# Kernel optimization log

Measured on AMD Instinct MI355X. Metric: run time of the kernel, lower is better.

## Reference

```python
import jax, jax.numpy as jnp
import numpy as np

NUM_USERS = 50000
NUM_ITEMS = 50000
NUM_CATS = 500
LATENT_DIM = 64
N_LAYERS = 3
N_EDGES = 500000
NNZ_G = 1000000
NNZ_GX = 2000000
BATCH = 8192
N_NODES = NUM_USERS + NUM_ITEMS


def _spmm(rows, cols, vals, x, n_out):
    # sparse COO matmul: out[r] += vals * x[c]
    return jax.ops.segment_sum(vals[:, None] * x[cols], rows, num_segments=n_out)


def setup_inputs() -> dict:
    key = jax.random.key(0)
    ks = jax.random.split(key, 14)
    return {
        "user_emb": 0.1 * jax.random.normal(ks[0], (NUM_USERS, LATENT_DIM), jnp.float32),
        "item_emb": 0.1 * jax.random.normal(ks[1], (NUM_ITEMS, LATENT_DIM), jnp.float32),
        "cat_emb": 0.1 * jax.random.normal(ks[2], (NUM_CATS, 2 * LATENT_DIM), jnp.float32),
        "g_vals": jax.random.uniform(ks[3], (NNZ_G,), jnp.float32),
        "gx_vals": jax.random.uniform(ks[4], (NNZ_GX,), jnp.float32),
        "g_rows": jax.random.randint(ks[5], (NNZ_G,), 0, N_NODES, jnp.int32),
        "g_cols": jax.random.randint(ks[6], (NNZ_G,), 0, N_NODES, jnp.int32),
        "gx_rows": jax.random.randint(ks[7], (NNZ_GX,), 0, N_EDGES, jnp.int32),
        "gx_cols": jax.random.randint(ks[8], (NNZ_GX,), 0, N_EDGES, jnp.int32),
        "train_users": jax.random.randint(ks[9], (N_EDGES,), 0, NUM_USERS, jnp.int32),
        "train_items": jax.random.randint(ks[10], (N_EDGES,), 0, NUM_ITEMS, jnp.int32),
        "item_to_category": jax.random.randint(ks[11], (NUM_ITEMS,), 0, NUM_CATS, jnp.int32),
        "users": jax.random.randint(ks[12], (BATCH,), 0, NUM_USERS, jnp.int32),
        "items": jax.random.randint(ks[13], (BATCH,), 0, NUM_ITEMS, jnp.int32),
    }


def _computer(user_emb, item_emb, cat_emb, g_rows, g_cols, g_vals,
              gx_rows, gx_cols, gx_vals, train_users, train_items, item_to_category):
    D = LATENT_DIM
    all_emb = jnp.concatenate([user_emb, item_emb], axis=0)  # [N, D]
    item_nodes = NUM_USERS + train_items  # [E]
    # degree = bincount over train_users and shifted train_items
    degree = (jnp.zeros((N_NODES,), all_emb.dtype)
              .at[train_users].add(1.0)
              .at[item_nodes].add(1.0))
    edge_cat = cat_emb[item_to_category[train_items]]  # [E, 2D]
    embs = []
    for i in range(N_LAYERS):
        all_emb = _spmm(g_rows, g_cols, g_vals, all_emb, N_NODES)  # [N, D]
        # edge features: user||item concat, +category emb on first layer
        feat = jnp.concatenate([all_emb[train_users], all_emb[item_nodes]], axis=-1)  # [E, 2D]
        if i == 0:
            feat = feat + edge_cat
        feat = _spmm(gx_rows, gx_cols, gx_vals, feat, N_EDGES)  # [E, 2D]
        # scatter edge halves back to nodes, degree-normalize, residual average
        upd = (jnp.zeros_like(all_emb)
               .at[train_users].add(feat[:, :D])
               .at[item_nodes].add(feat[:, D:]))
        upd = upd / (degree[:, None] + 1e-9)
        all_emb = (upd + all_emb) * 0.5
        embs.append(all_emb)
    light_out = jnp.mean(jnp.stack(embs, axis=1), axis=1)  # mean over layers 1..L
    return light_out[:NUM_USERS], light_out[NUM_USERS:]


def reference(user_emb, item_emb, cat_emb, g_vals, gx_vals, g_rows, g_cols,
              gx_rows, gx_cols, train_users, train_items, item_to_category,
              users, items):
    all_users, all_items = _computer(user_emb, item_emb, cat_emb,
                                     g_rows, g_cols, g_vals,
                                     gx_rows, gx_cols, gx_vals,
                                     train_users, train_items, item_to_category)
    u = all_users[users]   # [B, D]
    it = all_items[items]  # [B, D]
    gamma = jnp.sum(u * it, axis=1)  # [B]
    return gamma
```

## Files before the change

### kernel.cpp

```cpp
#include <hip/hip_runtime.h>

#define NUM_USERS 50000
#define NUM_ITEMS 50000
#define NUM_CATS  500
#define D         64
#define N_LAYERS  3
#define N_EDGES   500000
#define NNZ_G     1000000
#define NNZ_GX    2000000
#define BATCH     8192
#define N_NODES   (NUM_USERS + NUM_ITEMS)

#define BKT_SHIFT 4
#define BKT_W     16
#define NBKT      (N_NODES / BKT_W)

#define SB_SHIFT  9
#define SB_W      512
#define NSB       ((N_NODES + SB_W - 1) / SB_W)
#define P1_K      8
#define P1_TILE   (256 * P1_K)

__device__ __forceinline__ unsigned bf16rne(float f) {
    unsigned u = __float_as_uint(f);
    return (u + 0x7FFFu + ((u >> 16) & 1u)) >> 16;
}
__device__ __forceinline__ void bf16x8_to_f8(uint4 w, float* r) {
    r[0] = __uint_as_float(w.x << 16); r[1] = __uint_as_float(w.x & 0xFFFF0000u);
    r[2] = __uint_as_float(w.y << 16); r[3] = __uint_as_float(w.y & 0xFFFF0000u);
    r[4] = __uint_as_float(w.z << 16); r[5] = __uint_as_float(w.z & 0xFFFF0000u);
    r[6] = __uint_as_float(w.w << 16); r[7] = __uint_as_float(w.w & 0xFFFF0000u);
}
__device__ __forceinline__ uint4 f8_to_bf16x8(const float* r) {
    uint4 w;
    w.x = bf16rne(r[0]) | (bf16rne(r[1]) << 16);
    w.y = bf16rne(r[2]) | (bf16rne(r[3]) << 16);
    w.z = bf16rne(r[4]) | (bf16rne(r[5]) << 16);
    w.w = bf16rne(r[6]) | (bf16rne(r[7]) << 16);
    return w;
}

__global__ void init_deg_kernel(const float* __restrict__ ue, const float* __restrict__ ie,
                                const int* __restrict__ tu, const int* __restrict__ ti,
                                ushort* __restrict__ xb, float* __restrict__ deg) {
    int tid = blockIdx.x * blockDim.x + threadIdx.x;
    int stride = gridDim.x * blockDim.x;
    for (int e = tid; e < N_EDGES; e += stride) {
        unsafeAtomicAdd(deg + tu[e], 1.0f);
        unsafeAtomicAdd(deg + NUM_USERS + ti[e], 1.0f);
    }
    const int half = NUM_USERS * D / 4;
    for (int i4 = tid; i4 < N_NODES * D / 4; i4 += stride) {
        float4 v = (i4 < half) ? ((const float4*)ue)[i4] : ((const float4*)ie)[i4 - half];
        uint2 p;
        p.x = bf16rne(v.x) | (bf16rne(v.y) << 16);
        p.y = bf16rne(v.z) | (bf16rne(v.w) << 16);
        ((uint2*)xb)[i4] = p;
    }
}

__global__ void dinv_kernel(float* __restrict__ deg) {
    int n = blockIdx.x * blockDim.x + threadIdx.x;
    if (n < N_NODES) deg[n] = 1.0f / (deg[n] + 1e-9f);
}

__global__ void histsb_c_kernel(const int* __restrict__ gx_rows,
                                const int* __restrict__ tu, const int* __restrict__ ti,
                                int* __restrict__ cnt) {
    __shared__ int h[NSB];
    for (int i = threadIdx.x; i < NSB; i += blockDim.x) h[i] = 0;
    __syncthreads();
    int stride = gridDim.x * blockDim.x;
    for (int j = blockIdx.x * blockDim.x + threadIdx.x; j < NNZ_GX; j += stride) {
        int r = gx_rows[j];
        atomicAdd(h + (tu[r] >> SB_SHIFT), 1);
        atomicAdd(h + ((NUM_USERS + ti[r]) >> SB_SHIFT), 1);
    }
    __syncthreads();
    for (int i = threadIdx.x; i < NSB; i += blockDim.x)
        if (h[i]) atomicAdd(cnt + i, h[i]);
}

__global__ void scansb_kernel(const int* __restrict__ cnt, int* __restrict__ off,
                              int* __restrict__ cur, int* __restrict__ row_sentinel) {
    if (threadIdx.x == 0) {
        int run = 0;
        for (int i = 0; i < NSB; ++i) { off[i] = run; cur[i] = run; run += cnt[i]; }
        off[NSB] = run;
        row_sentinel[0] = run;
    }
}

__global__ void __launch_bounds__(256) p1c_kernel(
        const int* __restrict__ gx_rows, const int* __restrict__ gx_cols,
        const float* __restrict__ gx_vals,
        const int* __restrict__ tu, const int* __restrict__ ti,
        const int* __restrict__ i2c,
        int* __restrict__ sbcur, int2* __restrict__ out) {
    __shared__ int2 recs[2 * P1_TILE];
    __shared__ int h[NSB], base[NSB], cur[NSB];
    int t = threadIdx.x;
    for (int i = t; i < NSB; i += 256) { h[i] = 0; cur[i] = 0; }
    __syncthreads();
    int tb = blockIdx.x * P1_TILE;
    #pragma unroll
    for (int k = 0; k < P1_K; ++k) {
        int l = t + k * 256;
        int j = tb + l;
        if (j < NNZ_GX) {
            int r = gx_rows[j], c = gx_cols[j];
            unsigned vb = bf16rne(gx_vals[j]);
            int tur = tu[r], tir = ti[r], tuc = tu[c], tic = ti[c];
            int cat = i2c[tic];
            int ylo = (int)(vb << 16) | (cat << 1);
            unsigned dstu = (unsigned)tur;           int srcu = tuc;
            unsigned dsti = (unsigned)(NUM_USERS + tir); int srci = NUM_USERS + tic;
            recs[l] = make_int2((int)((dstu << 15) | (unsigned)(srcu & 0x7FFF)),
                                ylo | (((srcu >> 15) & 3) << 10));
            recs[P1_TILE + l] = make_int2((int)((dsti << 15) | (unsigned)(srci & 0x7FFF)),
                                          ylo | (((srci >> 15) & 3) << 10) | 1);
            atomicAdd(h + (int)(dstu >> SB_SHIFT), 1);
            atomicAdd(h + (int)(dsti >> SB_SHIFT), 1);
        }
    }
    __syncthreads();
    if (t < NSB) base[t] = atomicAdd(sbcur + t, h[t]);
    __syncthreads();
    int rem = NNZ_GX - tb;
    int nv = rem < P1_TILE ? rem : P1_TILE;
    for (int s = t; s < nv; s += 256) {
        int2 rec = recs[s];
        int bkt = (int)(((unsigned)rec.x) >> 24);
        int p = base[bkt] + atomicAdd(cur + bkt, 1);
        out[p] = rec;
        rec = recs[P1_TILE + s];
        bkt = (int)(((unsigned)rec.x) >> 24);
        p = base[bkt] + atomicAdd(cur + bkt, 1);
        out[p] = rec;
    }
}

__global__ void __launch_bounds__(512) p2c_kernel(
        const int* __restrict__ sboff, const int2* __restrict__ raw,
        int2* __restrict__ sorted, int* __restrict__ rowC) {
    int b = blockIdx.x;
    int beg = sboff[b], end = sboff[b + 1];
    __shared__ int h[SB_W], cur[SB_W];
    int t = threadIdx.x;
    h[t] = 0;
    __syncthreads();
    for (int i = beg + t; i < end; i += 512)
        atomicAdd(h + (int)((((unsigned)raw[i].x) >> 15) & (SB_W - 1)), 1);
    __syncthreads();
    int cnt = h[t];
    for (int o = 1; o < SB_W; o <<= 1) {
        int tmp = (t >= o) ? h[t - o] : 0;
        __syncthreads();
        h[t] += tmp;
        __syncthreads();
    }
    int excl = h[t] - cnt;
    cur[t] = beg + excl;
    int node = b * SB_W + t;
    if (node < N_NODES) rowC[node] = beg + excl;
    __syncthreads();
    for (int i = beg + t; i < end; i += 512) {
        int2 e = raw[i];
        unsigned rx = (unsigned)e.x;
        int dl = (int)((rx >> 15) & (SB_W - 1));
        int src = (int)(rx & 0x7FFF) | (((e.y >> 10) & 3) << 15);
        int p = atomicAdd(cur + dl, 1);
        sorted[p] = make_int2((src << 10) | (e.y & 0x3FF), e.y & 0xFFFF0000);
    }
}

__global__ void histg_kernel(const int* __restrict__ g_rows, int* __restrict__ cnt) {
    __shared__ int h[NBKT];
    for (int i = threadIdx.x; i < NBKT; i += blockDim.x) h[i] = 0;
    __syncthreads();
    int stride = gridDim.x * blockDim.x;
    for (int e = blockIdx.x * blockDim.x + threadIdx.x; e < NNZ_G; e += stride)
        atomicAdd(h + (g_rows[e] >> BKT_SHIFT), 1);
    __syncthreads();
    for (int i = threadIdx.x; i < NBKT; i += blockDim.x)
        if (h[i]) atomicAdd(cnt + i, h[i]);
}

__global__ void scang_kernel(const int* __restrict__ cnt, int* __restrict__ off,
                             int* __restrict__ cur, int* __restrict__ row) {
    __shared__ int sums[1024];
    const int T = 1024;
    const int strip = (NBKT + T - 1) / T;
    int t = threadIdx.x;
    int beg = t * strip;
    int end = beg + strip; if (end > NBKT) end = NBKT;
    int s = 0;
    for (int i = beg; i < end; ++i) s += cnt[i];
    sums[t] = s;
    __syncthreads();
    if (t == 0) {
        int run = 0;
        for (int i = 0; i < T; ++i) { int v = sums[i]; sums[i] = run; run += v; }
        off[NBKT] = run;
        row[N_NODES] = run;
    }
    __syncthreads();
    int run = sums[t];
    for (int i = beg; i < end; ++i) { off[i] = run; cur[i] = run; run += cnt[i]; }
}

__global__ void append_g_kernel(const int* __restrict__ g_rows, const int* __restrict__ g_cols,
                                const float* __restrict__ g_vals,
                                int* __restrict__ cur, int2* __restrict__ edges) {
    int e = blockIdx.x * blockDim.x + threadIdx.x;
    if (e >= NNZ_G) return;
    int dst = g_rows[e];
    int p = atomicAdd(cur + (dst >> BKT_SHIFT), 1);
    edges[p] = make_int2(((dst & (BKT_W - 1)) << 17) | g_cols[e], __float_as_int(g_vals[e]));
}

__global__ void sort_g_kernel(const int* __restrict__ off, const int2* __restrict__ raw,
                              int2* __restrict__ sorted, int* __restrict__ rowG) {
    int b = blockIdx.x;
    int base = off[b], end = off[b + 1];
    __shared__ int hist[BKT_W], cur[BKT_W], scn[BKT_W];
    if (threadIdx.x < BKT_W) hist[threadIdx.x] = 0;
    __syncthreads();
    for (int i = base + threadIdx.x; i < end; i += blockDim.x)
        atomicAdd(hist + ((raw[i].x >> 17) & 15), 1);
    __syncthreads();
    if (threadIdx.x == 0) {
        int run = 0;
        for (int k = 0; k < BKT_W; ++k) { scn[k] = run; cur[k] = run; run += hist[k]; }
    }
    __syncthreads();
    if (threadIdx.x < BKT_W) rowG[b * BKT_W + threadIdx.x] = base + scn[threadIdx.x];
    for (int i = base + threadIdx.x; i < end; i += blockDim.x) {
        int2 e = raw[i];
        int dl = (e.x >> 17) & 15;
        int p = atomicAdd(cur + dl, 1);
        sorted[base + p] = make_int2((e.x & 0x1FFFF) << 6, e.y);
    }
}

__global__ void pull_g_kernel(const int* __restrict__ row, const int2* __restrict__ edges,
                              const ushort* __restrict__ xb, ushort* __restrict__ tb) {
    int node = (blockIdx.x * blockDim.x + threadIdx.x) >> 5;
    int l32 = threadIdx.x & 31;
    if (node >= N_NODES) return;
    int g = l32 >> 3;
    int s = l32 & 7;
    int beg = row[node], end = row[node + 1];
    float acc[8] = {0.f, 0.f, 0.f, 0.f, 0.f, 0.f, 0.f, 0.f};
    #pragma unroll 2
    for (int i = beg + g; i < end; i += 4) {
        int2 e = edges[i];
        float v = __int_as_float(e.y);
        uint4 w = *(const uint4*)(xb + e.x + s * 8);
        float xv[8];
        bf16x8_to_f8(w, xv);
        #pragma unroll
        for (int d = 0; d < 8; ++d) acc[d] += v * xv[d];
    }
    #pragma unroll
    for (int d = 0; d < 8; ++d) {
        acc[d] += __shfl_xor(acc[d], 8, 64);
        acc[d] += __shfl_xor(acc[d], 16, 64);
    }
    if (l32 < 8) {
        uint4 p = f8_to_bf16x8(acc);
        *(uint4*)(tb + (size_t)node * D + s * 8) = p;
    }
}

template <int LAYER0>
__global__ void pull_c_fused(const int* __restrict__ row, const int2* __restrict__ edges,
                             const float* __restrict__ catbase,
                             const ushort* __restrict__ tb,
                             const float* __restrict__ dinv,
                             ushort* __restrict__ xout) {
    int node = (blockIdx.x * blockDim.x + threadIdx.x) >> 5;
    int l32 = threadIdx.x & 31;
    if (node >= N_NODES) return;
    int g = l32 >> 3;
    int s = l32 & 7;
    int beg = row[node], end = row[node + 1];
    float acc[8] = {0.f, 0.f, 0.f, 0.f, 0.f, 0.f, 0.f, 0.f};
    #pragma unroll 2
    for (int i = beg + g; i < end; i += 4) {
        int2 e = edges[i];
        float v = __int_as_float(e.y);
        int src = e.x >> 10;
        uint4 w = *(const uint4*)(tb + (size_t)src * D + s * 8);
        float xv[8];
        bf16x8_to_f8(w, xv);
        if (LAYER0) {
            int code = e.x & 1023;
            const float* cb = catbase + (code >> 1) * (2 * D) + ((code & 1) << 6) + s * 8;
            float4 c0 = *(const float4*)cb;
            float4 c1 = *(const float4*)(cb + 4);
            xv[0] += c0.x; xv[1] += c0.y; xv[2] += c0.z; xv[3] += c0.w;
            xv[4] += c1.x; xv[5] += c1.y; xv[6] += c1.z; xv[7] += c1.w;
        }
        #pragma unroll
        for (int d = 0; d < 8; ++d) acc[d] += v * xv[d];
    }
    #pragma unroll
    for (int d = 0; d < 8; ++d) {
        acc[d] += __shfl_xor(acc[d], 8, 64);
        acc[d] += __shfl_xor(acc[d], 16, 64);
    }
    if (l32 < 8) {
        float di = dinv[node];
        size_t o = (size_t)node * D + s * 8;
        uint4 tw = *(const uint4*)(tb + o);
        float tv[8];
        bf16x8_to_f8(tw, tv);
        float nx[8];
        #pragma unroll
        for (int d = 0; d < 8; ++d) nx[d] = (acc[d] * di + tv[d]) * 0.5f;
        *(uint4*)(xout + o) = f8_to_bf16x8(nx);
    }
}

__global__ void gamma3_kernel(const int* __restrict__ users, const int* __restrict__ items,
                              const ushort* __restrict__ x1, const ushort* __restrict__ x2,
                              const ushort* __restrict__ x3, float* __restrict__ out) {
    int wave = (blockIdx.x * blockDim.x + threadIdx.x) >> 6;
    int lane = threadIdx.x & 63;
    if (wave >= BATCH) return;
    size_t ou = (size_t)users[wave] * D + lane;
    size_t oi = (size_t)(NUM_USERS + items[wave]) * D + lane;
    float su = __uint_as_float((unsigned)x1[ou] << 16)
             + __uint_as_float((unsigned)x2[ou] << 16)
             + __uint_as_float((unsigned)x3[ou] << 16);
    float si = __uint_as_float((unsigned)x1[oi] << 16)
             + __uint_as_float((unsigned)x2[oi] << 16)
             + __uint_as_float((unsigned)x3[oi] << 16);
    float p = su * si;
#pragma unroll
    for (int off = 32; off > 0; off >>= 1) p += __shfl_down(p, off, 64);
    if (lane == 0) out[wave] = p * (1.0f / 9.0f);
}

extern "C" void kernel_launch(void* const* d_in, const int* in_sizes, int n_in,
                              void* d_out, int out_size, void* d_ws, size_t ws_size,
                              hipStream_t stream) {
    const float* user_emb = (const float*)d_in[0];
    const float* item_emb = (const float*)d_in[1];
    const float* cat_emb  = (const float*)d_in[2];
    const float* g_vals   = (const float*)d_in[3];
    const float* gx_vals  = (const float*)d_in[4];
    const int* g_rows  = (const int*)d_in[5];
    const int* g_cols  = (const int*)d_in[6];
    const int* gx_rows = (const int*)d_in[7];
    const int* gx_cols = (const int*)d_in[8];
    const int* train_users = (const int*)d_in[9];
    const int* train_items = (const int*)d_in[10];
    const int* i2c   = (const int*)d_in[11];
    const int* users = (const int*)d_in[12];
    const int* items = (const int*)d_in[13];
    float* out = (float*)d_out;

    char* ws = (char*)d_ws;
    size_t off = 0;
    auto alloc = [&](size_t bytes) -> void* {
        void* p = ws + off;
        off += (bytes + 255) & ~(size_t)255;
        return p;
    };
    const size_t NBH = (size_t)N_NODES * D * sizeof(ushort);
    ushort* x0b  = (ushort*)alloc(NBH);
    ushort* x1b  = (ushort*)alloc(NBH);
    ushort* x2b  = (ushort*)alloc(NBH);
    ushort* x3b  = (ushort*)alloc(NBH);
    ushort* tb   = (ushort*)alloc(NBH);
    float*  dinv = (float*)alloc((size_t)N_NODES * sizeof(float));
    int*  sbhC  = (int*)alloc((size_t)NSB * sizeof(int));
    int*  sboffC= (int*)alloc((size_t)(NSB + 1) * sizeof(int));
    int*  sbcurC= (int*)alloc((size_t)NSB * sizeof(int));
    int*  cntG  = (int*)alloc((size_t)NBKT * sizeof(int));
    int*  offG  = (int*)alloc((size_t)(NBKT + 1) * sizeof(int));
    int*  curG  = (int*)alloc((size_t)NBKT * sizeof(int));
    int*  rowC  = (int*)alloc((size_t)(N_NODES + 1) * sizeof(int));
    int*  rowG  = (int*)alloc((size_t)(N_NODES + 1) * sizeof(int));
    int2* edgeCr = (int2*)alloc((size_t)2 * NNZ_GX * sizeof(int2));
    int2* edgeCs = (int2*)alloc((size_t)2 * NNZ_GX * sizeof(int2));
    int2* edgeGr = (int2*)alloc((size_t)NNZ_G * sizeof(int2));
    int2* edgeGs = (int2*)alloc((size_t)NNZ_G * sizeof(int2));

    hipMemsetAsync(dinv, 0, (size_t)N_NODES * sizeof(float), stream);
    hipMemsetAsync(sbhC, 0, (size_t)NSB * sizeof(int), stream);
    hipMemsetAsync(cntG, 0, (size_t)NBKT * sizeof(int), stream);

    init_deg_kernel<<<4096, 256, 0, stream>>>(user_emb, item_emb, train_users, train_items,
                                              x0b, dinv);
    dinv_kernel<<<(N_NODES + 255) / 256, 256, 0, stream>>>(dinv);

    histsb_c_kernel<<<256, 256, 0, stream>>>(gx_rows, train_users, train_items, sbhC);
    scansb_kernel<<<1, 64, 0, stream>>>(sbhC, sboffC, sbcurC, rowC + N_NODES);
    p1c_kernel<<<(NNZ_GX + P1_TILE - 1) / P1_TILE, 256, 0, stream>>>(
        gx_rows, gx_cols, gx_vals, train_users, train_items, i2c, sbcurC, edgeCr);
    p2c_kernel<<<NSB, 512, 0, stream>>>(sboffC, edgeCr, edgeCs, rowC);

    histg_kernel<<<256, 256, 0, stream>>>(g_rows, cntG);
    scang_kernel<<<1, 1024, 0, stream>>>(cntG, offG, curG, rowG);
    append_g_kernel<<<(NNZ_G + 255) / 256, 256, 0, stream>>>(g_rows, g_cols, g_vals,
                                                             curG, edgeGr);
    sort_g_kernel<<<NBKT, 256, 0, stream>>>(offG, edgeGr, edgeGs, rowG);

    const int pull_grid = (N_NODES * 32 + 255) / 256;
    ushort* xin[4] = {x0b, x1b, x2b, x3b};
    for (int layer = 0; layer < N_LAYERS; ++layer) {
        pull_g_kernel<<<pull_grid, 256, 0, stream>>>(rowG, edgeGs, xin[layer], tb);
        if (layer == 0)
            pull_c_fused<1><<<pull_grid, 256, 0, stream>>>(rowC, edgeCs, cat_emb, tb,
                                                           dinv, xin[layer + 1]);
        else
            pull_c_fused<0><<<pull_grid, 256, 0, stream>>>(rowC, edgeCs, cat_emb, tb,
                                                           dinv, xin[layer + 1]);
    }

    gamma3_kernel<<<(BATCH * 64 + 255) / 256, 256, 0, stream>>>(users, items,
                                                                x1b, x2b, x3b, out);
}
```

Before: 680.5 us.

## Sort nodes by degree for pull kernels and merge histogram/scan launches

Adds a counting sort of nodes by their CSR row degree, producing permutations that the pull kernels use so each wavefront handles nodes of similar degree. This is meant to reduce load imbalance and divergence within a wave. It also merges the two histogram kernels and the two scan kernels into single launches, and raises the pull-loop unroll from 2 to 4. The cost is three extra small kernels, an indirect perm load per node, and loss of locality in output writes.

```diff
diff --git a/kernel.cpp b/kernel.cpp
--- a/kernel.cpp
+++ b/kernel.cpp
@@ -21,6 +21,8 @@
 #define P1_K      8
 #define P1_TILE   (256 * P1_K)
 
+#define MAXDEG    1024
+
 __device__ __forceinline__ unsigned bf16rne(float f) {
     unsigned u = __float_as_uint(f);
     return (u + 0x7FFFu + ((u >> 16) & 1u)) >> 16;
@@ -64,31 +66,64 @@
     if (n < N_NODES) deg[n] = 1.0f / (deg[n] + 1e-9f);
 }
 
-__global__ void histsb_c_kernel(const int* __restrict__ gx_rows,
-                                const int* __restrict__ tu, const int* __restrict__ ti,
-                                int* __restrict__ cnt) {
-    __shared__ int h[NSB];
-    for (int i = threadIdx.x; i < NSB; i += blockDim.x) h[i] = 0;
+__global__ void hist_both_kernel(const int* __restrict__ gx_rows,
+                                 const int* __restrict__ tu, const int* __restrict__ ti,
+                                 const int* __restrict__ g_rows,
+                                 int* __restrict__ cntC, int* __restrict__ cntG) {
+    __shared__ int hC[NSB];
+    __shared__ int hG[NBKT];
+    for (int i = threadIdx.x; i < NSB; i += blockDim.x) hC[i] = 0;
+    for (int i = threadIdx.x; i < NBKT; i += blockDim.x) hG[i] = 0;
     __syncthreads();
     int stride = gridDim.x * blockDim.x;
-    for (int j = blockIdx.x * blockDim.x + threadIdx.x; j < NNZ_GX; j += stride) {
+    int t0 = blockIdx.x * blockDim.x + threadIdx.x;
+    for (int j = t0; j < NNZ_GX; j += stride) {
         int r = gx_rows[j];
-        atomicAdd(h + (tu[r] >> SB_SHIFT), 1);
-        atomicAdd(h + ((NUM_USERS + ti[r]) >> SB_SHIFT), 1);
-    }
+        atomicAdd(hC + (tu[r] >> SB_SHIFT), 1);
+        atomicAdd(hC + ((NUM_USERS + ti[r]) >> SB_SHIFT), 1);
+    }
+    for (int e = t0; e < NNZ_G; e += stride)
+        atomicAdd(hG + (g_rows[e] >> BKT_SHIFT), 1);
     __syncthreads();
     for (int i = threadIdx.x; i < NSB; i += blockDim.x)
-        if (h[i]) atomicAdd(cnt + i, h[i]);
-}
-
-__global__ void scansb_kernel(const int* __restrict__ cnt, int* __restrict__ off,
-                              int* __restrict__ cur, int* __restrict__ row_sentinel) {
-    if (threadIdx.x == 0) {
+        if (hC[i]) atomicAdd(cntC + i, hC[i]);
+    for (int i = threadIdx.x; i < NBKT; i += blockDim.x)
+        if (hG[i]) atomicAdd(cntG + i, hG[i]);
+}
+
+__global__ void __launch_bounds__(1024) scan2_kernel(
+        const int* __restrict__ cntC, int* __restrict__ offC, int* __restrict__ curC,
+        int* __restrict__ rowC,
+        const int* __restrict__ cntG, int* __restrict__ offG, int* __restrict__ curG,
+        int* __restrict__ rowG) {
+    if (blockIdx.x == 0) {
+        if (threadIdx.x == 0) {
+            int run = 0;
+            for (int i = 0; i < NSB; ++i) { offC[i] = run; curC[i] = run; run += cntC[i]; }
+            offC[NSB] = run;
+            rowC[N_NODES] = run;
+        }
+        return;
+    }
+    __shared__ int sums[1024];
+    const int T = 1024;
+    const int strip = (NBKT + T - 1) / T;
+    int t = threadIdx.x;
+    int beg = t * strip;
+    int end = beg + strip; if (end > NBKT) end = NBKT;
+    int s = 0;
+    for (int i = beg; i < end; ++i) s += cntG[i];
+    sums[t] = s;
+    __syncthreads();
+    if (t == 0) {
         int run = 0;
-        for (int i = 0; i < NSB; ++i) { off[i] = run; cur[i] = run; run += cnt[i]; }
-        off[NSB] = run;
-        row_sentinel[0] = run;
-    }
+        for (int i = 0; i < T; ++i) { int v = sums[i]; sums[i] = run; run += v; }
+        offG[NBKT] = run;
+        rowG[N_NODES] = run;
+    }
+    __syncthreads();
+    int run = sums[t];
+    for (int i = beg; i < end; ++i) { offG[i] = run; curG[i] = run; run += cntG[i]; }
 }
 
 __global__ void __launch_bounds__(256) p1c_kernel(
@@ -174,41 +209,6 @@
     }
 }
 
-__global__ void histg_kernel(const int* __restrict__ g_rows, int* __restrict__ cnt) {
-    __shared__ int h[NBKT];
-    for (int i = threadIdx.x; i < NBKT; i += blockDim.x) h[i] = 0;
-    __syncthreads();
-    int stride = gridDim.x * blockDim.x;
-    for (int e = blockIdx.x * blockDim.x + threadIdx.x; e < NNZ_G; e += stride)
-        atomicAdd(h + (g_rows[e] >> BKT_SHIFT), 1);
-    __syncthreads();
-    for (int i = threadIdx.x; i < NBKT; i += blockDim.x)
-        if (h[i]) atomicAdd(cnt + i, h[i]);
-}
-
-__global__ void scang_kernel(const int* __restrict__ cnt, int* __restrict__ off,
-                             int* __restrict__ cur, int* __restrict__ row) {
-    __shared__ int sums[1024];
-    const int T = 1024;
-    const int strip = (NBKT + T - 1) / T;
-    int t = threadIdx.x;
-    int beg = t * strip;
-    int end = beg + strip; if (end > NBKT) end = NBKT;
-    int s = 0;
-    for (int i = beg; i < end; ++i) s += cnt[i];
-    sums[t] = s;
-    __syncthreads();
-    if (t == 0) {
-        int run = 0;
-        for (int i = 0; i < T; ++i) { int v = sums[i]; sums[i] = run; run += v; }
-        off[NBKT] = run;
-        row[N_NODES] = run;
-    }
-    __syncthreads();
-    int run = sums[t];
-    for (int i = beg; i < end; ++i) { off[i] = run; cur[i] = run; run += cnt[i]; }
-}
-
 __global__ void append_g_kernel(const int* __restrict__ g_rows, const int* __restrict__ g_cols,
                                 const float* __restrict__ g_vals,
                                 int* __restrict__ cur, int2* __restrict__ edges) {
@@ -243,16 +243,72 @@
     }
 }
 
-__global__ void pull_g_kernel(const int* __restrict__ row, const int2* __restrict__ edges,
+__global__ void deghist_kernel(const int* __restrict__ rowC, const int* __restrict__ rowG,
+                               int* __restrict__ gHC, int* __restrict__ gHG) {
+    __shared__ int hC[MAXDEG], hG[MAXDEG];
+    int t = threadIdx.x;
+    for (int i = t; i < MAXDEG; i += blockDim.x) { hC[i] = 0; hG[i] = 0; }
+    __syncthreads();
+    int stride = gridDim.x * blockDim.x;
+    for (int n = blockIdx.x * blockDim.x + t; n < N_NODES; n += stride) {
+        int dC = rowC[n + 1] - rowC[n]; dC = dC < MAXDEG ? dC : MAXDEG - 1;
+        atomicAdd(hC + dC, 1);
+        int dG = rowG[n + 1] - rowG[n]; dG = dG < MAXDEG ? dG : MAXDEG - 1;
+        atomicAdd(hG + dG, 1);
+    }
+    __syncthreads();
+    for (int i = t; i < MAXDEG; i += blockDim.x) {
+        if (hC[i]) atomicAdd(gHC + i, hC[i]);
+        if (hG[i]) atomicAdd(gHG + i, hG[i]);
+    }
+}
+
+__global__ void __launch_bounds__(1024) degscan_kernel(int* __restrict__ gHC,
+                                                       int* __restrict__ gHG) {
+    __shared__ int part[1024];
+    int t = threadIdx.x;
+    int c = gHC[t];
+    part[t] = c;
+    __syncthreads();
+    for (int o = 1; o < 1024; o <<= 1) {
+        int v = (t >= o) ? part[t - o] : 0;
+        __syncthreads(); part[t] += v; __syncthreads();
+    }
+    gHC[t] = part[t] - c;
+    int g = gHG[t];
+    __syncthreads();
+    part[t] = g;
+    __syncthreads();
+    for (int o = 1; o < 1024; o <<= 1) {
+        int v = (t >= o) ? part[t - o] : 0;
+        __syncthreads(); part[t] += v; __syncthreads();
+    }
+    gHG[t] = part[t] - g;
+}
+
+__global__ void degplace_kernel(const int* __restrict__ rowC, const int* __restrict__ rowG,
+                                int* __restrict__ gHC, int* __restrict__ gHG,
+                                int* __restrict__ permC, int* __restrict__ permG) {
+    int n = blockIdx.x * blockDim.x + threadIdx.x;
+    if (n >= N_NODES) return;
+    int dC = rowC[n + 1] - rowC[n]; dC = dC < MAXDEG ? dC : MAXDEG - 1;
+    permC[atomicAdd(gHC + dC, 1)] = n;
+    int dG = rowG[n + 1] - rowG[n]; dG = dG < MAXDEG ? dG : MAXDEG - 1;
+    permG[atomicAdd(gHG + dG, 1)] = n;
+}
+
+__global__ void pull_g_kernel(const int* __restrict__ row, const int* __restrict__ perm,
+                              const int2* __restrict__ edges,
                               const ushort* __restrict__ xb, ushort* __restrict__ tb) {
-    int node = (blockIdx.x * blockDim.x + threadIdx.x) >> 5;
+    int hw = (blockIdx.x * blockDim.x + threadIdx.x) >> 5;
     int l32 = threadIdx.x & 31;
-    if (node >= N_NODES) return;
+    if (hw >= N_NODES) return;
+    int node = perm[hw];
     int g = l32 >> 3;
     int s = l32 & 7;
     int beg = row[node], end = row[node + 1];
     float acc[8] = {0.f, 0.f, 0.f, 0.f, 0.f, 0.f, 0.f, 0.f};
-    #pragma unroll 2
+    #pragma unroll 4
     for (int i = beg + g; i < end; i += 4) {
         int2 e = edges[i];
         float v = __int_as_float(e.y);
@@ -274,19 +330,21 @@
 }
 
 template <int LAYER0>
-__global__ void pull_c_fused(const int* __restrict__ row, const int2* __restrict__ edges,
+__global__ void pull_c_fused(const int* __restrict__ row, const int* __restrict__ perm,
+                             const int2* __restrict__ edges,
                              const float* __restrict__ catbase,
                              const ushort* __restrict__ tb,
                              const float* __restrict__ dinv,
                              ushort* __restrict__ xout) {
-    int node = (blockIdx.x * blockDim.x + threadIdx.x) >> 5;
+    int hw = (blockIdx.x * blockDim.x + threadIdx.x) >> 5;
     int l32 = threadIdx.x & 31;
-    if (node >= N_NODES) return;
+    if (hw >= N_NODES) return;
+    int node = perm[hw];
     int g = l32 >> 3;
     int s = l32 & 7;
     int beg = row[node], end = row[node + 1];
     float acc[8] = {0.f, 0.f, 0.f, 0.f, 0.f, 0.f, 0.f, 0.f};
-    #pragma unroll 2
+    #pragma unroll 4
     for (int i = beg + g; i < end; i += 4) {
         int2 e = edges[i];
         float v = __int_as_float(e.y);
@@ -384,6 +442,10 @@
     int*  curG  = (int*)alloc((size_t)NBKT * sizeof(int));
     int*  rowC  = (int*)alloc((size_t)(N_NODES + 1) * sizeof(int));
     int*  rowG  = (int*)alloc((size_t)(N_NODES + 1) * sizeof(int));
+    int*  gHC   = (int*)alloc((size_t)MAXDEG * sizeof(int));
+    int*  gHG   = (int*)alloc((size_t)MAXDEG * sizeof(int));
+    int*  permC = (int*)alloc((size_t)N_NODES * sizeof(int));
+    int*  permG = (int*)alloc((size_t)N_NODES * sizeof(int));
     int2* edgeCr = (int2*)alloc((size_t)2 * NNZ_GX * sizeof(int2));
     int2* edgeCs = (int2*)alloc((size_t)2 * NNZ_GX * sizeof(int2));
     int2* edgeGr = (int2*)alloc((size_t)NNZ_G * sizeof(int2));
@@ -392,32 +454,40 @@
     hipMemsetAsync(dinv, 0, (size_t)N_NODES * sizeof(float), stream);
     hipMemsetAsync(sbhC, 0, (size_t)NSB * sizeof(int), stream);
     hipMemsetAsync(cntG, 0, (size_t)NBKT * sizeof(int), stream);
+    hipMemsetAsync(gHC, 0, (size_t)MAXDEG * sizeof(int), stream);
+    hipMemsetAsync(gHG, 0, (size_t)MAXDEG * sizeof(int), stream);
 
     init_deg_kernel<<<4096, 256, 0, stream>>>(user_emb, item_emb, train_users, train_items,
                                               x0b, dinv);
     dinv_kernel<<<(N_NODES + 255) / 256, 256, 0, stream>>>(dinv);
 
-    histsb_c_kernel<<<256, 256, 0, stream>>>(gx_rows, train_users, train_items, sbhC);
-    scansb_kernel<<<1, 64, 0, stream>>>(sbhC, sboffC, sbcurC, rowC + N_NODES);
+    hist_both_kernel<<<256, 256, 0, stream>>>(gx_rows, train_users, train_items, g_rows,
+                                              sbhC, cntG);
+    scan2_kernel<<<2, 1024, 0, stream>>>(sbhC, sboffC, sbcurC, rowC,
+                                         cntG, offG, curG, rowG);
+
     p1c_kernel<<<(NNZ_GX + P1_TILE - 1) / P1_TILE, 256, 0, stream>>>(
         gx_rows, gx_cols, gx_vals, train_users, train_items, i2c, sbcurC, edgeCr);
     p2c_kernel<<<NSB, 512, 0, stream>>>(sboffC, edgeCr, edgeCs, rowC);
 
-    histg_kernel<<<256, 256, 0, stream>>>(g_rows, cntG);
-    scang_kernel<<<1, 1024, 0, stream>>>(cntG, offG, curG, rowG);
     append_g_kernel<<<(NNZ_G + 255) / 256, 256, 0, stream>>>(g_rows, g_cols, g_vals,
                                                              curG, edgeGr);
     sort_g_kernel<<<NBKT, 256, 0, stream>>>(offG, edgeGr, edgeGs, rowG);
 
+    deghist_kernel<<<128, 256, 0, stream>>>(rowC, rowG, gHC, gHG);
+    degscan_kernel<<<1, 1024, 0, stream>>>(gHC, gHG);
+    degplace_kernel<<<(N_NODES + 255) / 256, 256, 0, stream>>>(rowC, rowG, gHC, gHG,
+                                                               permC, permG);
+
     const int pull_grid = (N_NODES * 32 + 255) / 256;
     ushort* xin[4] = {x0b, x1b, x2b, x3b};
     for (int layer = 0; layer < N_LAYERS; ++layer) {
-        pull_g_kernel<<<pull_grid, 256, 0, stream>>>(rowG, edgeGs, xin[layer], tb);
+        pull_g_kernel<<<pull_grid, 256, 0, stream>>>(rowG, permG, edgeGs, xin[layer], tb);
         if (layer == 0)
-            pull_c_fused<1><<<pull_grid, 256, 0, stream>>>(rowC, edgeCs, cat_emb, tb,
+            pull_c_fused<1><<<pull_grid, 256, 0, stream>>>(rowC, permC, edgeCs, cat_emb, tb,
                                                            dinv, xin[layer + 1]);
         else
-            pull_c_fused<0><<<pull_grid, 256, 0, stream>>>(rowC, edgeCs, cat_emb, tb,
+            pull_c_fused<0><<<pull_grid, 256, 0, stream>>>(rowC, permC, edgeCs, cat_emb, tb,
                                                            dinv, xin[layer + 1]);
     }
 
```

After: 1.159 ms. 70.3% more time.
